# Kernel optimization log

Hardware: AMD Instinct MI355X
Metric: run time of the kernel (lower is better)

The kernel has to match this reference:

```python
import jax, jax.numpy as jnp
import numpy as np

NH, NP, NL, ED = 8, 8, 1, 256  # num_heads, num_sam_pts, num_levels, embed_dim
EPS = 1e-5


def setup_inputs() -> dict:
    key = jax.random.key(0)
    ks = jax.random.split(key, 6)
    bs, h, w = 8, 64, 64
    d = ED // NH
    return {
        "query": jax.random.normal(ks[0], (bs, 1, ED), jnp.float32),
        "single_feat": jax.random.normal(ks[1], (bs, h * w, NH, d), jnp.float32),
        "ref_2d": jax.random.uniform(ks[2], (bs, h * w, NL, 2), jnp.float32),
        "W_off": jax.random.normal(ks[3], (ED, NH * NL * NP * 2), jnp.float32) * 0.02,
        "b_off": jnp.zeros((NH * NL * NP * 2,), jnp.float32),
        "W_attn": jax.random.normal(ks[4], (ED, NH * NL * NP), jnp.float32) * 0.02,
        "b_attn": jnp.zeros((NH * NL * NP,), jnp.float32),
        "ln_g": jnp.ones((ED,), jnp.float32),
        "ln_b": jnp.zeros((ED,), jnp.float32),
        "h": h,
        "w": w,
    }


def reference(query, single_feat, ref_2d, W_off, b_off, W_attn, b_attn, ln_g, ln_b, h, w):
    bs, nq, _, d = single_feat.shape
    # query: [bs,1,ED] repeated over all h*w query positions
    q = jnp.broadcast_to(query, (bs, h * w, ED))

    # sampling offsets (relu'd, normalized by (w,h)) added to reference points
    off = jax.nn.relu(q @ W_off + b_off).reshape(bs, nq, NH, NL, NP, 2)
    offset_normalizer = jnp.array([w, h], dtype=q.dtype)  # (w, h) order as in torch
    loc = ref_2d[:, :, None, :, None, :] + off / offset_normalizer  # [bs,nq,NH,NL,NP,2]

    # attention weights: relu then softmax over points (last axis)
    aw = jax.nn.relu(q @ W_attn + b_attn).reshape(bs, nq, NH, NL, NP)
    aw = jax.nn.softmax(aw, axis=-1)

    # single-level bilinear grid_sample (align_corners=False, zero padding)
    g = 2.0 * loc[:, :, :, 0] - 1.0  # level 0 -> [bs,nq,NH,NP,2]
    x = (g[..., 0] + 1.0) * (w / 2.0) - 0.5  # pixel coords
    y = (g[..., 1] + 1.0) * (h / 2.0) - 0.5
    x0 = jnp.floor(x)
    y0 = jnp.floor(y)
    x0i = x0.astype(jnp.int32)
    y0i = y0.astype(jnp.int32)

    v = single_feat.transpose(0, 2, 1, 3)  # [bs,NH,H*W,d]

    def gather(xi, yi):
        valid = (xi >= 0) & (xi < w) & (yi >= 0) & (yi < h)  # [bs,nq,NH,NP]
        idx = jnp.clip(yi, 0, h - 1) * w + jnp.clip(xi, 0, w - 1)
        idx = idx.transpose(0, 2, 1, 3).reshape(bs, NH, nq * NP, 1)
        s = jnp.take_along_axis(v, idx, axis=2).reshape(bs, NH, nq, NP, d)
        return s * valid.transpose(0, 2, 1, 3)[..., None].astype(s.dtype)

    wx = (x - x0).transpose(0, 2, 1, 3)[..., None]  # [bs,NH,nq,NP,1]
    wy = (y - y0).transpose(0, 2, 1, 3)[..., None]
    s00 = gather(x0i, y0i)
    s01 = gather(x0i + 1, y0i)
    s10 = gather(x0i, y0i + 1)
    s11 = gather(x0i + 1, y0i + 1)
    top = s00 * (1.0 - wx) + s01 * wx
    bot = s10 * (1.0 - wx) + s11 * wx
    sampled = top * (1.0 - wy) + bot * wy  # [bs,NH,nq,NP,d]

    # weighted sum over points, merge heads
    out = jnp.einsum('bhqpd,bqhp->bqhd', sampled, aw[:, :, :, 0]).reshape(bs, nq, NH * d)

    # norm(dropout(output) + query) -- dropout is identity in eval mode
    res = out + q
    mu = res.mean(-1, keepdims=True)
    var = res.var(-1, keepdims=True)
    return (res - mu) / jnp.sqrt(var + EPS) * ln_g + ln_b
```

## Files before the change

### kernel.cpp

```cpp
#include <hip/hip_runtime.h>

#define ED 256
#define NHEAD 8
#define NPTS 8
#define DHEAD 32
#define QPB 8

typedef _Float16 half8v __attribute__((ext_vector_type(8)));

__global__ __launch_bounds__(256) void convert_kernel(
    const float4* __restrict__ feat, half8v* __restrict__ feat16,
    int per_batch8, int bs)
{
    const int b      = blockIdx.x % bs;
    const int chunk  = blockIdx.x / bs;
    const int nchunk = gridDim.x / bs;
    const size_t base = (size_t)b * per_batch8;

    for (int i = chunk * 256 + threadIdx.x; i < per_batch8; i += nchunk * 256) {
        const size_t idx = base + i;
        const float4 f0 = feat[2 * idx];
        const float4 f1 = feat[2 * idx + 1];
        half8v h;
        h[0] = (_Float16)f0.x; h[1] = (_Float16)f0.y;
        h[2] = (_Float16)f0.z; h[3] = (_Float16)f0.w;
        h[4] = (_Float16)f1.x; h[5] = (_Float16)f1.y;
        h[6] = (_Float16)f1.z; h[7] = (_Float16)f1.w;
        feat16[idx] = h;
    }
}

__global__ __launch_bounds__(256) void precompute_kernel(
    const float* __restrict__ query,
    const float* __restrict__ W_off, const float* __restrict__ b_off,
    const float* __restrict__ W_attn, const float* __restrict__ b_attn,
    float* __restrict__ ws)
{
    const int b = blockIdx.x;
    const int t = threadIdx.x;
    __shared__ float sq[ED];
    __shared__ float red[256];
    __shared__ float sattn[64];

    sq[t] = query[b * ED + t];
    __syncthreads();

    {
        const int col  = t & 127;
        const int half = t >> 7;
        const float* Wp = W_off + (size_t)half * 128 * 128 + col;
        const float* qp = sq + half * 128;
        float a0 = 0.f, a1 = 0.f, a2 = 0.f, a3 = 0.f;
        #pragma unroll 8
        for (int k = 0; k < 128; k += 4) {
            a0 = fmaf(qp[k + 0], Wp[(k + 0) * 128], a0);
            a1 = fmaf(qp[k + 1], Wp[(k + 1) * 128], a1);
            a2 = fmaf(qp[k + 2], Wp[(k + 2) * 128], a2);
            a3 = fmaf(qp[k + 3], Wp[(k + 3) * 128], a3);
        }
        red[t] = (a0 + a1) + (a2 + a3);
    }
    __syncthreads();
    if (t < 128) ws[b * 192 + t] = fmaxf(red[t] + red[t + 128] + b_off[t], 0.0f);
    __syncthreads();

    {
        const int col = t & 63;
        const int qtr = t >> 6;
        const float* Wp = W_attn + (size_t)qtr * 64 * 64 + col;
        const float* qp = sq + qtr * 64;
        float a0 = 0.f, a1 = 0.f, a2 = 0.f, a3 = 0.f;
        #pragma unroll 8
        for (int k = 0; k < 64; k += 4) {
            a0 = fmaf(qp[k + 0], Wp[(k + 0) * 64], a0);
            a1 = fmaf(qp[k + 1], Wp[(k + 1) * 64], a1);
            a2 = fmaf(qp[k + 2], Wp[(k + 2) * 64], a2);
            a3 = fmaf(qp[k + 3], Wp[(k + 3) * 64], a3);
        }
        red[t] = (a0 + a1) + (a2 + a3);
    }
    __syncthreads();
    if (t < 64) {
        sattn[t] = fmaxf(red[t] + red[t + 64] + red[t + 128] + red[t + 192]
                         + b_attn[t], 0.0f);
    }
    __syncthreads();
    if (t < 64) {
        const int hh = t >> 3;
        float m = -1e30f;
        #pragma unroll
        for (int p = 0; p < NPTS; ++p) m = fmaxf(m, sattn[hh * NPTS + p]);
        float s = 0.0f;
        #pragma unroll
        for (int p = 0; p < NPTS; ++p) s += expf(sattn[hh * NPTS + p] - m);
        ws[b * 192 + 128 + t] = expf(sattn[t] - m) / s;
    }
}

__global__ __launch_bounds__(256, 6) void deform_attn_kernel(
    const _Float16* __restrict__ feat16,
    const float* __restrict__ ref2d,
    const float* __restrict__ query,
    const float* __restrict__ ln_g, const float* __restrict__ ln_b,
    const float* __restrict__ ws,
    const int* __restrict__ Hp, const int* __restrict__ Wp,
    float* __restrict__ out,
    int nq, int bs)
{
    const int blk = blockIdx.x;
    const int b = blk % bs;
    const int qbase = (blk / bs) * QPB;
    const int t = threadIdx.x;

    __shared__ float s_off[128];
    __shared__ float s_aw[64];
    __shared__ float s_ref[QPB * 2];
    __shared__ uint4  s_ofs[QPB * 64];
    __shared__ float4 s_wt [QPB * 64];

    if (t < 128)      s_off[t] = ws[b * 192 + t];
    else if (t < 192) s_aw[t - 128] = ws[b * 192 + t];
    else if (t < 192 + QPB * 2) {
        const int i = t - 192;
        s_ref[i] = ref2d[(b * nq + qbase + (i >> 1)) * 2 + (i & 1)];
    }
    const int H = Hp[0];
    const int W = Wp[0];
    __syncthreads();

    #pragma unroll
    for (int u = t; u < QPB * 64; u += 256) {
        const int qL = u >> 6;
        const int l  = u & 63;
        const int p  = l >> 3;
        const int h  = l & 7;
        const int hp = h * 8 + p;

        const float x = s_ref[qL * 2 + 0] * (float)W - 0.5f + s_off[hp * 2 + 0];
        const float y = s_ref[qL * 2 + 1] * (float)H - 0.5f + s_off[hp * 2 + 1];
        const float aw = s_aw[hp];

        const float xf = floorf(x);
        const float yf = floorf(y);
        const int ix = (int)xf;
        const int iy = (int)yf;
        const float wx = x - xf;
        const float wy = y - yf;

        const bool vx0 = (ix >= 0) && (ix < W);
        const bool vx1 = (ix + 1 >= 0) && (ix + 1 < W);
        const bool vy0 = (iy >= 0) && (iy < H);
        const bool vy1 = (iy + 1 >= 0) && (iy + 1 < H);
        const int cx0 = min(max(ix, 0), W - 1);
        const int cx1 = min(max(ix + 1, 0), W - 1);
        const int cy0 = min(max(iy, 0), H - 1);
        const int cy1 = min(max(iy + 1, 0), H - 1);

        const int r0 = cy0 * W;
        const int r1 = cy1 * W;
        uint4 ofs;
        ofs.x = (unsigned)(r0 + cx0) << 9;
        ofs.y = (unsigned)(r0 + cx1) << 9;
        ofs.z = (unsigned)(r1 + cx0) << 9;
        ofs.w = (unsigned)(r1 + cx1) << 9;

        const float awx = aw * wx, awix = aw - awx;
        float4 wt;
        wt.x = (vx0 && vy0) ? awix * (1.0f - wy) : 0.0f;
        wt.y = (vx1 && vy0) ? awx  * (1.0f - wy) : 0.0f;
        wt.z = (vx0 && vy1) ? awix * wy          : 0.0f;
        wt.w = (vx1 && vy1) ? awx  * wy          : 0.0f;

        s_ofs[u] = ofs;
        s_wt[u]  = wt;
    }
    __syncthreads();

    const int wave = t >> 6;
    const int lane = t & 63;
    const int half = lane >> 5;
    const int l32  = lane & 31;
    const int h    = l32 >> 2;
    const int c16  = l32 & 3;
    const int qloc = wave * 2 + half;
    const int q    = qbase + qloc;
    const int cb   = qloc * 64 + h;

    const char* fb = (const char*)feat16 + (size_t)b * nq * (NHEAD * DHEAD * 2);
    const unsigned laneofs = (unsigned)(h * 64 + c16 * 16);

    float acc[8] = {0.f, 0.f, 0.f, 0.f, 0.f, 0.f, 0.f, 0.f};

    #pragma unroll
    for (int pp = 0; pp < NPTS; pp += 2) {
        const uint4  iA = s_ofs[cb + pp * 8];
        const float4 wA = s_wt [cb + pp * 8];
        const uint4  iB = s_ofs[cb + pp * 8 + 8];
        const float4 wB = s_wt [cb + pp * 8 + 8];

        const half8v a0 = *(const half8v*)(fb + (iA.x + laneofs));
        const half8v a1 = *(const half8v*)(fb + (iA.y + laneofs));
        const half8v a2 = *(const half8v*)(fb + (iA.z + laneofs));
        const half8v a3 = *(const half8v*)(fb + (iA.w + laneofs));
        const half8v b0 = *(const half8v*)(fb + (iB.x + laneofs));
        const half8v b1 = *(const half8v*)(fb + (iB.y + laneofs));
        const half8v b2 = *(const half8v*)(fb + (iB.z + laneofs));
        const half8v b3 = *(const half8v*)(fb + (iB.w + laneofs));

        #pragma unroll
        for (int j = 0; j < 8; ++j) {
            acc[j] = fmaf(wA.x, (float)a0[j], acc[j]);
            acc[j] = fmaf(wA.y, (float)a1[j], acc[j]);
            acc[j] = fmaf(wA.z, (float)a2[j], acc[j]);
            acc[j] = fmaf(wA.w, (float)a3[j], acc[j]);
            acc[j] = fmaf(wB.x, (float)b0[j], acc[j]);
            acc[j] = fmaf(wB.y, (float)b1[j], acc[j]);
            acc[j] = fmaf(wB.z, (float)b2[j], acc[j]);
            acc[j] = fmaf(wB.w, (float)b3[j], acc[j]);
        }
    }

    const float4 qv0 = *(const float4*)(query + b * ED + l32 * 8);
    const float4 qv1 = *(const float4*)(query + b * ED + l32 * 8 + 4);
    float r[8];
    r[0] = acc[0] + qv0.x; r[1] = acc[1] + qv0.y;
    r[2] = acc[2] + qv0.z; r[3] = acc[3] + qv0.w;
    r[4] = acc[4] + qv1.x; r[5] = acc[5] + qv1.y;
    r[6] = acc[6] + qv1.z; r[7] = acc[7] + qv1.w;

    float s = 0.f, ss = 0.f;
    #pragma unroll
    for (int j = 0; j < 8; ++j) {
        s += r[j];
        ss = fmaf(r[j], r[j], ss);
    }
    #pragma unroll
    for (int m = 1; m < 32; m <<= 1) {
        s  += __shfl_xor(s, m, 64);
        ss += __shfl_xor(ss, m, 64);
    }
    const float mean = s * (1.0f / ED);
    const float var  = ss * (1.0f / ED) - mean * mean;
    const float inv  = rsqrtf(var + 1e-5f);

    const float4 g0  = *(const float4*)(ln_g + l32 * 8);
    const float4 g1  = *(const float4*)(ln_g + l32 * 8 + 4);
    const float4 be0 = *(const float4*)(ln_b + l32 * 8);
    const float4 be1 = *(const float4*)(ln_b + l32 * 8 + 4);

    float4 o0, o1;
    o0.x = (r[0] - mean) * inv * g0.x + be0.x;
    o0.y = (r[1] - mean) * inv * g0.y + be0.y;
    o0.z = (r[2] - mean) * inv * g0.z + be0.z;
    o0.w = (r[3] - mean) * inv * g0.w + be0.w;
    o1.x = (r[4] - mean) * inv * g1.x + be1.x;
    o1.y = (r[5] - mean) * inv * g1.y + be1.y;
    o1.z = (r[6] - mean) * inv * g1.z + be1.z;
    o1.w = (r[7] - mean) * inv * g1.w + be1.w;

    float* op = out + ((size_t)b * nq + q) * ED + l32 * 8;
    *(float4*)op       = o0;
    *(float4*)(op + 4) = o1;
}

extern "C" void kernel_launch(void* const* d_in, const int* in_sizes, int n_in,
                              void* d_out, int out_size, void* d_ws, size_t ws_size,
                              hipStream_t stream)
{
    const float* query  = (const float*)d_in[0];
    const float* feat   = (const float*)d_in[1];
    const float* ref2d  = (const float*)d_in[2];
    const float* W_off  = (const float*)d_in[3];
    const float* b_off  = (const float*)d_in[4];
    const float* W_attn = (const float*)d_in[5];
    const float* b_attn = (const float*)d_in[6];
    const float* ln_g   = (const float*)d_in[7];
    const float* ln_b   = (const float*)d_in[8];
    const int*   Hp     = (const int*)d_in[9];
    const int*   Wp     = (const int*)d_in[10];
    float* out = (float*)d_out;
    float* ws  = (float*)d_ws;

    const int bs = in_sizes[0] / ED;
    const int nq = in_sizes[2] / (bs * 2);
    const int nfeat = in_sizes[1];
    const int per_batch8 = nfeat / (bs * 8);

    _Float16* feat16 = (_Float16*)((char*)d_ws + 8192);

    convert_kernel<<<bs * 256, 256, 0, stream>>>((const float4*)feat,
                                                 (half8v*)feat16, per_batch8, bs);
    precompute_kernel<<<bs, 256, 0, stream>>>(query, W_off, b_off, W_attn, b_attn, ws);
    deform_attn_kernel<<<bs * nq / QPB, 256, 0, stream>>>((const _Float16*)feat16,
                                                          ref2d, query, ln_g, ln_b,
                                                          ws, Hp, Wp, out, nq, bs);
}
```

Measured before the change: 138.1 us.

## Merge convert and precompute kernels, software-pipeline gathers in deform kernel

Folds the fp16 conversion and the offset/attention-weight precompute into one launch, with the first bs blocks doing the precompute, which removes one kernel launch and its serialization. The gather loop in the deform kernel is restructured into explicit issue/consume stages separated by sched_barriers, so the next two points' loads are in flight while the current ones are accumulated. LayerNorm parameter loads are hoisted ahead of the loop, and launch bounds drop from 6 to 4 waves per SIMD to leave room for the extra registers. The cost is lower occupancy and more register pressure in exchange for more memory-level parallelism per wave.

```diff
diff --git a/kernel.cpp b/kernel.cpp
--- a/kernel.cpp
+++ b/kernel.cpp
@@ -8,36 +8,37 @@
 
 typedef _Float16 half8v __attribute__((ext_vector_type(8)));
 
-__global__ __launch_bounds__(256) void convert_kernel(
+__global__ __launch_bounds__(256) void prep_kernel(
     const float4* __restrict__ feat, half8v* __restrict__ feat16,
-    int per_batch8, int bs)
-{
-    const int b      = blockIdx.x % bs;
-    const int chunk  = blockIdx.x / bs;
-    const int nchunk = gridDim.x / bs;
-    const size_t base = (size_t)b * per_batch8;
-
-    for (int i = chunk * 256 + threadIdx.x; i < per_batch8; i += nchunk * 256) {
-        const size_t idx = base + i;
-        const float4 f0 = feat[2 * idx];
-        const float4 f1 = feat[2 * idx + 1];
-        half8v h;
-        h[0] = (_Float16)f0.x; h[1] = (_Float16)f0.y;
-        h[2] = (_Float16)f0.z; h[3] = (_Float16)f0.w;
-        h[4] = (_Float16)f1.x; h[5] = (_Float16)f1.y;
-        h[6] = (_Float16)f1.z; h[7] = (_Float16)f1.w;
-        feat16[idx] = h;
-    }
-}
-
-__global__ __launch_bounds__(256) void precompute_kernel(
+    int per_batch8,
     const float* __restrict__ query,
     const float* __restrict__ W_off, const float* __restrict__ b_off,
     const float* __restrict__ W_attn, const float* __restrict__ b_attn,
-    float* __restrict__ ws)
+    float* __restrict__ ws, int bs)
 {
+    const int t = threadIdx.x;
+
+    if ((int)blockIdx.x >= bs) {
+        const int cid    = blockIdx.x - bs;
+        const int b      = cid % bs;
+        const int chunk  = cid / bs;
+        const int nchunk = (gridDim.x - bs) / bs;
+        const size_t base = (size_t)b * per_batch8;
+        for (int i = chunk * 256 + t; i < per_batch8; i += nchunk * 256) {
+            const size_t idx = base + i;
+            const float4 f0 = feat[2 * idx];
+            const float4 f1 = feat[2 * idx + 1];
+            half8v h;
+            h[0] = (_Float16)f0.x; h[1] = (_Float16)f0.y;
+            h[2] = (_Float16)f0.z; h[3] = (_Float16)f0.w;
+            h[4] = (_Float16)f1.x; h[5] = (_Float16)f1.y;
+            h[6] = (_Float16)f1.z; h[7] = (_Float16)f1.w;
+            feat16[idx] = h;
+        }
+        return;
+    }
+
     const int b = blockIdx.x;
-    const int t = threadIdx.x;
     __shared__ float sq[ED];
     __shared__ float red[256];
     __shared__ float sattn[64];
@@ -97,7 +98,7 @@
     }
 }
 
-__global__ __launch_bounds__(256, 6) void deform_attn_kernel(
+__global__ __launch_bounds__(256, 4) void deform_attn_kernel(
     const _Float16* __restrict__ feat16,
     const float* __restrict__ ref2d,
     const float* __restrict__ query,
@@ -189,39 +190,57 @@
     const char* fb = (const char*)feat16 + (size_t)b * nq * (NHEAD * DHEAD * 2);
     const unsigned laneofs = (unsigned)(h * 64 + c16 * 16);
 
-    float acc[8] = {0.f, 0.f, 0.f, 0.f, 0.f, 0.f, 0.f, 0.f};
-
-    #pragma unroll
-    for (int pp = 0; pp < NPTS; pp += 2) {
-        const uint4  iA = s_ofs[cb + pp * 8];
-        const float4 wA = s_wt [cb + pp * 8];
-        const uint4  iB = s_ofs[cb + pp * 8 + 8];
-        const float4 wB = s_wt [cb + pp * 8 + 8];
-
-        const half8v a0 = *(const half8v*)(fb + (iA.x + laneofs));
-        const half8v a1 = *(const half8v*)(fb + (iA.y + laneofs));
-        const half8v a2 = *(const half8v*)(fb + (iA.z + laneofs));
-        const half8v a3 = *(const half8v*)(fb + (iA.w + laneofs));
-        const half8v b0 = *(const half8v*)(fb + (iB.x + laneofs));
-        const half8v b1 = *(const half8v*)(fb + (iB.y + laneofs));
-        const half8v b2 = *(const half8v*)(fb + (iB.z + laneofs));
-        const half8v b3 = *(const half8v*)(fb + (iB.w + laneofs));
-
-        #pragma unroll
-        for (int j = 0; j < 8; ++j) {
-            acc[j] = fmaf(wA.x, (float)a0[j], acc[j]);
-            acc[j] = fmaf(wA.y, (float)a1[j], acc[j]);
-            acc[j] = fmaf(wA.z, (float)a2[j], acc[j]);
-            acc[j] = fmaf(wA.w, (float)a3[j], acc[j]);
-            acc[j] = fmaf(wB.x, (float)b0[j], acc[j]);
-            acc[j] = fmaf(wB.y, (float)b1[j], acc[j]);
-            acc[j] = fmaf(wB.z, (float)b2[j], acc[j]);
-            acc[j] = fmaf(wB.w, (float)b3[j], acc[j]);
-        }
-    }
-
     const float4 qv0 = *(const float4*)(query + b * ED + l32 * 8);
     const float4 qv1 = *(const float4*)(query + b * ED + l32 * 8 + 4);
+    const float4 g0  = *(const float4*)(ln_g + l32 * 8);
+    const float4 g1  = *(const float4*)(ln_g + l32 * 8 + 4);
+    const float4 be0 = *(const float4*)(ln_b + l32 * 8);
+    const float4 be1 = *(const float4*)(ln_b + l32 * 8 + 4);
+
+    float acc[8] = {0.f, 0.f, 0.f, 0.f, 0.f, 0.f, 0.f, 0.f};
+
+#define ISSUE(P, pp) \
+    const uint4  iA##P = s_ofs[cb + (pp) * 8]; \
+    const float4 wA##P = s_wt [cb + (pp) * 8]; \
+    const uint4  iB##P = s_ofs[cb + (pp) * 8 + 8]; \
+    const float4 wB##P = s_wt [cb + (pp) * 8 + 8]; \
+    const half8v A0##P = *(const half8v*)(fb + (iA##P.x + laneofs)); \
+    const half8v A1##P = *(const half8v*)(fb + (iA##P.y + laneofs)); \
+    const half8v A2##P = *(const half8v*)(fb + (iA##P.z + laneofs)); \
+    const half8v A3##P = *(const half8v*)(fb + (iA##P.w + laneofs)); \
+    const half8v B0##P = *(const half8v*)(fb + (iB##P.x + laneofs)); \
+    const half8v B1##P = *(const half8v*)(fb + (iB##P.y + laneofs)); \
+    const half8v B2##P = *(const half8v*)(fb + (iB##P.z + laneofs)); \
+    const half8v B3##P = *(const half8v*)(fb + (iB##P.w + laneofs));
+
+#define CONSUME(P) \
+    _Pragma("unroll") \
+    for (int j = 0; j < 8; ++j) { \
+        acc[j] = fmaf(wA##P.x, (float)A0##P[j], acc[j]); \
+        acc[j] = fmaf(wA##P.y, (float)A1##P[j], acc[j]); \
+        acc[j] = fmaf(wA##P.z, (float)A2##P[j], acc[j]); \
+        acc[j] = fmaf(wA##P.w, (float)A3##P[j], acc[j]); \
+        acc[j] = fmaf(wB##P.x, (float)B0##P[j], acc[j]); \
+        acc[j] = fmaf(wB##P.y, (float)B1##P[j], acc[j]); \
+        acc[j] = fmaf(wB##P.z, (float)B2##P[j], acc[j]); \
+        acc[j] = fmaf(wB##P.w, (float)B3##P[j], acc[j]); \
+    }
+
+    ISSUE(0, 0)
+    ISSUE(1, 2)
+    __builtin_amdgcn_sched_barrier(0);
+    CONSUME(0)
+    ISSUE(2, 4)
+    __builtin_amdgcn_sched_barrier(0);
+    CONSUME(1)
+    ISSUE(3, 6)
+    __builtin_amdgcn_sched_barrier(0);
+    CONSUME(2)
+    CONSUME(3)
+
+#undef ISSUE
+#undef CONSUME
+
     float r[8];
     r[0] = acc[0] + qv0.x; r[1] = acc[1] + qv0.y;
     r[2] = acc[2] + qv0.z; r[3] = acc[3] + qv0.w;
@@ -242,11 +261,6 @@
     const float mean = s * (1.0f / ED);
     const float var  = ss * (1.0f / ED) - mean * mean;
     const float inv  = rsqrtf(var + 1e-5f);
-
-    const float4 g0  = *(const float4*)(ln_g + l32 * 8);
-    const float4 g1  = *(const float4*)(ln_g + l32 * 8 + 4);
-    const float4 be0 = *(const float4*)(ln_b + l32 * 8);
-    const float4 be1 = *(const float4*)(ln_b + l32 * 8 + 4);
 
     float4 o0, o1;
     o0.x = (r[0] - mean) * inv * g0.x + be0.x;
@@ -288,9 +302,9 @@
 
     _Float16* feat16 = (_Float16*)((char*)d_ws + 8192);
 
-    convert_kernel<<<bs * 256, 256, 0, stream>>>((const float4*)feat,
-                                                 (half8v*)feat16, per_batch8, bs);
-    precompute_kernel<<<bs, 256, 0, stream>>>(query, W_off, b_off, W_attn, b_attn, ws);
+    prep_kernel<<<bs + bs * 256, 256, 0, stream>>>(
+        (const float4*)feat, (half8v*)feat16, per_batch8,
+        query, W_off, b_off, W_attn, b_attn, ws, bs);
     deform_attn_kernel<<<bs * nq / QPB, 256, 0, stream>>>((const _Float16*)feat16,
                                                           ref2d, query, ln_g, ln_b,
                                                           ws, Hp, Wp, out, nq, bs);
```

After: 134.1 us. 2.9% less time.
